# Kernel optimization log

Hardware: AMD Instinct MI355X
Metric: run time of the kernel (lower is better)

The kernel has to match this reference:

```python
import jax, jax.numpy as jnp
import numpy as np

NUM_HEADS = 8
NUM_POINTS = 9


def _bilinear_sample(img, gx, gy):
    """grid_sample, mode=bilinear, padding=zeros, align_corners=True.
    img: (B, C, H, W); gx, gy: (B, M) pixel coords. Returns (B, C, M)."""
    Bc, C, H, W = img.shape
    imgf = img.reshape(Bc, C, H * W)
    x0 = jnp.floor(gx)
    y0 = jnp.floor(gy)
    wx1 = gx - x0
    wy1 = gy - y0

    def corner(xi, yi, w):
        valid = (xi >= 0) & (xi < W) & (yi >= 0) & (yi < H)
        xi_c = jnp.clip(xi, 0, W - 1).astype(jnp.int32)
        yi_c = jnp.clip(yi, 0, H - 1).astype(jnp.int32)
        idx = yi_c * W + xi_c  # (B, M)
        g = jax.vmap(lambda im, ix: im[:, ix])(imgf, idx)  # (B, C, M)
        return g * (w * valid)[:, None, :]

    return (corner(x0, y0, (1 - wx1) * (1 - wy1))
            + corner(x0 + 1, y0, wx1 * (1 - wy1))
            + corner(x0, y0 + 1, (1 - wx1) * wy1)
            + corner(x0 + 1, y0 + 1, wx1 * wy1))


def setup_inputs() -> dict:
    key = jax.random.key(0)
    ks = jax.random.split(key, 6)
    B, Hp, Wp, T, D = 4, 64, 64, 3, 256
    N = Hp * Wp
    Hh, P = NUM_HEADS, NUM_POINTS
    x = jax.random.normal(ks[0], (B, N, T, D), dtype=jnp.float32)
    # offset/attn projections: small random (orig inits them to 0, which is degenerate for testing)
    W_off = jax.random.normal(ks[1], (D, Hh * P * 2), dtype=jnp.float32) * 0.01
    b_off = jnp.zeros((Hh * P * 2,), dtype=jnp.float32)
    W_attn = jax.random.normal(ks[2], (D, Hh * P), dtype=jnp.float32) * 0.01
    b_attn = jnp.zeros((Hh * P,), dtype=jnp.float32)
    W_v = jax.random.normal(ks[3], (D, D), dtype=jnp.float32) * 0.02
    b_v = jnp.zeros((D,), dtype=jnp.float32)
    W_o = jax.random.normal(ks[4], (D, D), dtype=jnp.float32) * 0.02
    b_o = jnp.zeros((D,), dtype=jnp.float32)
    return {"x": x, "W_off": W_off, "b_off": b_off, "W_attn": W_attn,
            "b_attn": b_attn, "W_v": W_v, "b_v": b_v, "W_o": W_o,
            "b_o": b_o, "Hp": Hp, "Wp": Wp}


def reference(x, W_off, b_off, W_attn, b_attn, W_v, b_v, W_o, b_o, Hp, Wp):
    B, N, T, D = x.shape
    Hh, P = NUM_HEADS, NUM_POINTS
    dh = D // Hh

    query = x[:, :, T // 2]  # (B, N, D) middle frame
    offset = (query @ W_off + b_off).reshape(B, N, Hh, P, 2)
    attn = jax.nn.softmax((query @ W_attn + b_attn).reshape(B, N, Hh, P), axis=-1)

    # reference points in [-1, 1], xy order (x = width coord)
    gh, gw = jnp.meshgrid(jnp.arange(Hp, dtype=jnp.float32),
                          jnp.arange(Wp, dtype=jnp.float32), indexing='ij')
    ref = jnp.stack([gw, gh], axis=-1).reshape(N, 2)
    ref = ref / jnp.asarray([Wp - 1, Hp - 1], dtype=jnp.float32) * 2 - 1

    loc = ref[None, :, None, None, :] + offset  # (B, N, H, P, 2) normalized

    value = (x @ W_v + b_v).reshape(B, N, T, Hh, dh)
    # (B, H, T, dh, N) -> (B*H*T, dh, Hp, Wp)
    val = jnp.transpose(value, (0, 3, 2, 4, 1)).reshape(B * Hh * T, dh, Hp, Wp)

    # per-(b,h) grid, shared across frames; fold T into batch of the sampler
    grid = jnp.transpose(loc, (0, 2, 1, 3, 4))  # (B, H, N, P, 2)
    grid = jnp.broadcast_to(grid[:, :, None], (B, Hh, T, N, P, 2))
    grid = grid.reshape(B * Hh * T, N * P, 2)
    gx = (grid[..., 0] + 1) * 0.5 * (Wp - 1)
    gy = (grid[..., 1] + 1) * 0.5 * (Hp - 1)

    sampled = _bilinear_sample(val, gx, gy)  # (B*H*T, dh, N*P)
    sampled = sampled.reshape(B, Hh, T, dh, N, P)

    # weighted sum over points, summed over frames
    out = jnp.einsum('bhtdnp,bnhp->bnhd', sampled, attn).reshape(B, N, D)
    return out @ W_o + b_o
```

## Files before the change

kernel.cpp:

```cpp
#include <hip/hip_runtime.h>
#include <hip/hip_bf16.h>


#define NH_ 8
#define DH_ 32
#define MM_ 16384

typedef __attribute__((ext_vector_type(8))) short bf16x8;
typedef __attribute__((ext_vector_type(4))) short bf16x4;
typedef __attribute__((ext_vector_type(4))) float f32x4;

static __device__ __forceinline__ unsigned short f2bf(float f) {
  unsigned int u = __float_as_uint(f);
  u = (u + 0x7fff + ((u >> 16) & 1)) >> 16;
  return (unsigned short)u;
}
static __device__ __forceinline__ float bf2f(unsigned short h) {
  return __uint_as_float(((unsigned int)h) << 16);
}

__global__ __launch_bounds__(256) void prep(
    const float* __restrict__ x,
    const float* __restrict__ W_off, const float* __restrict__ W_attn,
    const float* __restrict__ W_v, const float* __restrict__ W_o,
    const float* __restrict__ b_off, const float* __restrict__ b_attn,
    unsigned short* __restrict__ ash, unsigned short* __restrict__ asl,
    unsigned short* __restrict__ xmh, unsigned short* __restrict__ xml,
    unsigned short* __restrict__ wvh, unsigned short* __restrict__ wvl,
    unsigned short* __restrict__ wch, unsigned short* __restrict__ wcl,
    unsigned short* __restrict__ woh, unsigned short* __restrict__ wol,
    float* __restrict__ bcat) {
  const int bid = blockIdx.x, t = threadIdx.x;
  if (bid < 4096) {
    const int gid = bid * 256 + t;
    const int row = gid >> 6, c4 = (gid & 63) * 4;
    const float* xr = x + (size_t)row * 768 + c4;
    float4 a0 = *(const float4*)xr;
    float4 a1 = *(const float4*)(xr + 256);
    float4 a2 = *(const float4*)(xr + 512);
    float s[4] = {a0.x + a1.x + a2.x, a0.y + a1.y + a2.y,
                  a0.z + a1.z + a2.z, a0.w + a1.w + a2.w};
    float m[4] = {a1.x, a1.y, a1.z, a1.w};
    bf16x4 shv, slv, mhv, mlv;
#pragma unroll
    for (int j = 0; j < 4; ++j) {
      unsigned short h = f2bf(s[j]);
      shv[j] = (short)h; slv[j] = (short)f2bf(s[j] - bf2f(h));
      unsigned short h2 = f2bf(m[j]);
      mhv[j] = (short)h2; mlv[j] = (short)f2bf(m[j] - bf2f(h2));
    }
    const size_t o = (size_t)row * 256 + c4;
    *(bf16x4*)(ash + o) = shv;  *(bf16x4*)(asl + o) = slv;
    *(bf16x4*)(xmh + o) = mhv;  *(bf16x4*)(xml + o) = mlv;
  } else {
    const int n = bid - 4096;
    {
      float v = W_v[(size_t)t * 256 + n];
      unsigned short h = f2bf(v);
      wvh[n * 256 + t] = h; wvl[n * 256 + t] = f2bf(v - bf2f(h));
    }
    {
      float v = W_o[(size_t)t * 256 + n];
      unsigned short h = f2bf(v);
      woh[n * 256 + t] = h; wol[n * 256 + t] = f2bf(v - bf2f(h));
    }
    if (n < 216) {
      float v = (n < 144) ? W_off[(size_t)t * 144 + n] : W_attn[(size_t)t * 72 + (n - 144)];
      unsigned short h = f2bf(v);
      wch[n * 256 + t] = h; wcl[n * 256 + t] = f2bf(v - bf2f(h));
    }
    if (n == 0 && t < 216) bcat[t] = (t < 144) ? b_off[t] : b_attn[t - 144];
  }
}

__global__ __launch_bounds__(256) void mgemm01(
    const unsigned short* __restrict__ Ahi, const unsigned short* __restrict__ Alo,
    const unsigned short* __restrict__ Xmh, const unsigned short* __restrict__ Xml,
    const unsigned short* __restrict__ Wvh, const unsigned short* __restrict__ Wvl,
    const unsigned short* __restrict__ Wch, const unsigned short* __restrict__ Wcl,
    const float* __restrict__ b_v, const float* __restrict__ bcat,
    float* __restrict__ valsum, float* __restrict__ proj) {
  __shared__ unsigned short Ah[64][64], Al[64][64], Bh[128][64], Bl[128][64];
  const int mode1 = (blockIdx.y >= 2);
  const int n0 = (blockIdx.y & 1) * 128;
  const int m0 = blockIdx.x * 64;
  const int tid = threadIdx.x;
  const int wid = tid >> 6, lane = tid & 63;
  const int am = (wid >> 1) * 32, bn = (wid & 1) * 64;
  const int fr = lane & 15, kg = lane >> 4;
  const unsigned short* Asrch = mode1 ? Xmh : Ahi;
  const unsigned short* Asrcl = mode1 ? Xml : Alo;
  const unsigned short* Bth = mode1 ? Wch : Wvh;
  const unsigned short* Btl = mode1 ? Wcl : Wvl;

  f32x4 acc[2][4];
#pragma unroll
  for (int i = 0; i < 2; ++i)
#pragma unroll
    for (int j = 0; j < 4; ++j) acc[i][j] = (f32x4)(0.f);

  for (int k0 = 0; k0 < 256; k0 += 64) {
#pragma unroll
    for (int i = 0; i < 2; ++i) {
      int cid = i * 256 + tid;
      int r = cid >> 3, c = cid & 7;
      int dst = r * 64 + ((c ^ (r & 7)) * 8);
      size_t off = (size_t)(m0 + r) * 256 + k0 + c * 8;
      *(bf16x8*)(&Ah[0][0] + dst) = *(const bf16x8*)(Asrch + off);
      *(bf16x8*)(&Al[0][0] + dst) = *(const bf16x8*)(Asrcl + off);
    }
#pragma unroll
    for (int i = 0; i < 4; ++i) {
      int cid = i * 256 + tid;
      int r = cid >> 3, c = cid & 7;
      int dst = r * 64 + ((c ^ (r & 7)) * 8);
      int nrow = n0 + r;
      bf16x8 hv = (bf16x8)(short)0, lv = (bf16x8)(short)0;
      if (!mode1 || nrow < 216) {
        size_t off = (size_t)nrow * 256 + k0 + c * 8;
        hv = *(const bf16x8*)(Bth + off);
        lv = *(const bf16x8*)(Btl + off);
      }
      *(bf16x8*)(&Bh[0][0] + dst) = hv;
      *(bf16x8*)(&Bl[0][0] + dst) = lv;
    }
    __syncthreads();

#pragma unroll
    for (int ks = 0; ks < 2; ++ks) {
      const int kc = ks * 4 + kg;
      bf16x8 ah[2], al[2], bh[4], bl[4];
#pragma unroll
      for (int mi = 0; mi < 2; ++mi) {
        int m = am + mi * 16 + fr;
        int o = m * 64 + ((kc ^ (m & 7)) * 8);
        ah[mi] = *(const bf16x8*)(&Ah[0][0] + o);
        al[mi] = *(const bf16x8*)(&Al[0][0] + o);
      }
#pragma unroll
      for (int ni = 0; ni < 4; ++ni) {
        int n = bn + ni * 16 + fr;
        int o = n * 64 + ((kc ^ (n & 7)) * 8);
        bh[ni] = *(const bf16x8*)(&Bh[0][0] + o);
        bl[ni] = *(const bf16x8*)(&Bl[0][0] + o);
      }
#pragma unroll
      for (int mi = 0; mi < 2; ++mi)
#pragma unroll
        for (int ni = 0; ni < 4; ++ni) {
          acc[mi][ni] = __builtin_amdgcn_mfma_f32_16x16x32_bf16(ah[mi], bh[ni], acc[mi][ni], 0, 0, 0);
          acc[mi][ni] = __builtin_amdgcn_mfma_f32_16x16x32_bf16(ah[mi], bl[ni], acc[mi][ni], 0, 0, 0);
          acc[mi][ni] = __builtin_amdgcn_mfma_f32_16x16x32_bf16(al[mi], bh[ni], acc[mi][ni], 0, 0, 0);
        }
    }
    __syncthreads();
  }

  const int ro = kg * 4;
#pragma unroll
  for (int mi = 0; mi < 2; ++mi)
#pragma unroll
    for (int ni = 0; ni < 4; ++ni) {
      int col = n0 + bn + ni * 16 + fr;
      if (mode1 && col >= 216) continue;
      int rowb = m0 + am + mi * 16 + ro;
      float bv = mode1 ? bcat[col] : b_v[col] * 3.f;
#pragma unroll
      for (int r = 0; r < 4; ++r) {
        int grow = rowb + r;
        float v = acc[mi][ni][r] + bv;
        if (mode1) {
          proj[(size_t)grow * 216 + col] = v;
        } else {
          int b = grow >> 12, nn = grow & 4095;
          int h = col >> 5, d = col & 31;
          valsum[(((size_t)(b * NH_ + h) << 12) + nn) * DH_ + d] = v;
        }
      }
    }
}

__global__ __launch_bounds__(256) void mgemm2(
    const unsigned short* __restrict__ Ahi, const unsigned short* __restrict__ Alo,
    const unsigned short* __restrict__ Bth, const unsigned short* __restrict__ Btl,
    const float* __restrict__ bias, float* __restrict__ Cout) {
  __shared__ unsigned short Ah[64][64], Al[64][64], Bh[128][64], Bl[128][64];
  const int n0 = blockIdx.y * 128;
  const int m0 = blockIdx.x * 64;
  const int tid = threadIdx.x;
  const int wid = tid >> 6, lane = tid & 63;
  const int am = (wid >> 1) * 32, bn = (wid & 1) * 64;
  const int fr = lane & 15, kg = lane >> 4;

  f32x4 acc[2][4];
#pragma unroll
  for (int i = 0; i < 2; ++i)
#pragma unroll
    for (int j = 0; j < 4; ++j) acc[i][j] = (f32x4)(0.f);

  for (int k0 = 0; k0 < 256; k0 += 64) {
#pragma unroll
    for (int i = 0; i < 2; ++i) {
      int cid = i * 256 + tid;
      int r = cid >> 3, c = cid & 7;
      int dst = r * 64 + ((c ^ (r & 7)) * 8);
      size_t off = (size_t)(m0 + r) * 256 + k0 + c * 8;
      *(bf16x8*)(&Ah[0][0] + dst) = *(const bf16x8*)(Ahi + off);
      *(bf16x8*)(&Al[0][0] + dst) = *(const bf16x8*)(Alo + off);
    }
#pragma unroll
    for (int i = 0; i < 4; ++i) {
      int cid = i * 256 + tid;
      int r = cid >> 3, c = cid & 7;
      int dst = r * 64 + ((c ^ (r & 7)) * 8);
      size_t off = (size_t)(n0 + r) * 256 + k0 + c * 8;
      *(bf16x8*)(&Bh[0][0] + dst) = *(const bf16x8*)(Bth + off);
      *(bf16x8*)(&Bl[0][0] + dst) = *(const bf16x8*)(Btl + off);
    }
    __syncthreads();

#pragma unroll
    for (int ks = 0; ks < 2; ++ks) {
      const int kc = ks * 4 + kg;
      bf16x8 ah[2], al[2], bh[4], bl[4];
#pragma unroll
      for (int mi = 0; mi < 2; ++mi) {
        int m = am + mi * 16 + fr;
        int o = m * 64 + ((kc ^ (m & 7)) * 8);
        ah[mi] = *(const bf16x8*)(&Ah[0][0] + o);
        al[mi] = *(const bf16x8*)(&Al[0][0] + o);
      }
#pragma unroll
      for (int ni = 0; ni < 4; ++ni) {
        int n = bn + ni * 16 + fr;
        int o = n * 64 + ((kc ^ (n & 7)) * 8);
        bh[ni] = *(const bf16x8*)(&Bh[0][0] + o);
        bl[ni] = *(const bf16x8*)(&Bl[0][0] + o);
      }
#pragma unroll
      for (int mi = 0; mi < 2; ++mi)
#pragma unroll
        for (int ni = 0; ni < 4; ++ni) {
          acc[mi][ni] = __builtin_amdgcn_mfma_f32_16x16x32_bf16(ah[mi], bh[ni], acc[mi][ni], 0, 0, 0);
          acc[mi][ni] = __builtin_amdgcn_mfma_f32_16x16x32_bf16(ah[mi], bl[ni], acc[mi][ni], 0, 0, 0);
          acc[mi][ni] = __builtin_amdgcn_mfma_f32_16x16x32_bf16(al[mi], bh[ni], acc[mi][ni], 0, 0, 0);
        }
    }
    __syncthreads();
  }

  const int ro = kg * 4;
#pragma unroll
  for (int mi = 0; mi < 2; ++mi)
#pragma unroll
    for (int ni = 0; ni < 4; ++ni) {
      int col = n0 + bn + ni * 16 + fr;
      int rowb = m0 + am + mi * 16 + ro;
      float bv = bias[col];
#pragma unroll
      for (int r = 0; r < 4; ++r)
        Cout[(size_t)(rowb + r) * 256 + col] = acc[mi][ni][r] + bv;
    }
}

__global__ __launch_bounds__(256) void sample4(const float* __restrict__ valsum,
                                               const float* __restrict__ proj,
                                               unsigned short* __restrict__ ihi,
                                               unsigned short* __restrict__ ilo) {
  const int bid = blockIdx.x;
  const int wv = threadIdx.x >> 6;
  const int lane = threadIdx.x & 63;
  const int row = ((bid & 7) << 11) + ((bid >> 3) << 2) + wv;
  const int b = row >> 12, n = row & 4095;

  __shared__ int cidx[4][72][4];
  __shared__ float cw[4][72][4];
  __shared__ float sa[4][72];

  const float* pr = proj + (size_t)row * 216;
  for (int e = lane; e < 72; e += 64) {
    float ox = pr[e * 2], oy = pr[e * 2 + 1];
    float gx = (float)(n & 63) + ox * 31.5f;
    float gy = (float)(n >> 6) + oy * 31.5f;
    float fx0 = floorf(gx), fy0 = floorf(gy);
    float wx1 = gx - fx0, wy1 = gy - fy0;
    float wx0 = 1.f - wx1, wy0 = 1.f - wy1;
    int x0 = (int)fx0, y0 = (int)fy0, x1 = x0 + 1, y1 = y0 + 1;
    bool vx0 = (x0 >= 0) & (x0 < 64), vx1 = (x1 >= 0) & (x1 < 64);
    bool vy0 = (y0 >= 0) & (y0 < 64), vy1 = (y1 >= 0) & (y1 < 64);
    int x0c = min(max(x0, 0), 63), x1c = min(max(x1, 0), 63);
    int y0c = min(max(y0, 0), 63), y1c = min(max(y1, 0), 63);
    cidx[wv][e][0] = (y0c * 64 + x0c) * DH_; cw[wv][e][0] = (vx0 & vy0) ? wx0 * wy0 : 0.f;
    cidx[wv][e][1] = (y0c * 64 + x1c) * DH_; cw[wv][e][1] = (vx1 & vy0) ? wx1 * wy0 : 0.f;
    cidx[wv][e][2] = (y1c * 64 + x0c) * DH_; cw[wv][e][2] = (vx0 & vy1) ? wx0 * wy1 : 0.f;
    cidx[wv][e][3] = (y1c * 64 + x1c) * DH_; cw[wv][e][3] = (vx1 & vy1) ? wx1 * wy1 : 0.f;
  }
  if (lane < 8) {
    const float* pa = pr + 144 + lane * 9;
    float lg[9], mx = -1e30f;
#pragma unroll
    for (int p = 0; p < 9; ++p) { lg[p] = pa[p]; mx = fmaxf(mx, lg[p]); }
    float s = 0.f;
#pragma unroll
    for (int p = 0; p < 9; ++p) { lg[p] = __expf(lg[p] - mx); s += lg[p]; }
    float inv = 1.f / s;
#pragma unroll
    for (int p = 0; p < 9; ++p) sa[wv][lane * 9 + p] = lg[p] * inv;
  }
  __syncthreads();

  const int h = lane >> 3, d4 = (lane & 7) * 4;
  const float* vb = valsum + ((size_t)((b * NH_ + h) << 12)) * DH_ + d4;
  float ax = 0.f, ay = 0.f, az = 0.f, aw = 0.f;
#pragma unroll
  for (int p = 0; p < 9; ++p) {
    const int hp = h * 9 + p;
    float sx = 0.f, sy = 0.f, sz = 0.f, sw = 0.f;
#pragma unroll
    for (int c = 0; c < 4; ++c) {
      float4 v = *(const float4*)(vb + cidx[wv][hp][c]);
      float w = cw[wv][hp][c];
      sx += w * v.x; sy += w * v.y; sz += w * v.z; sw += w * v.w;
    }
    float ap = sa[wv][hp];
    ax += ap * sx; ay += ap * sy; az += ap * sz; aw += ap * sw;
  }
  float av[4] = {ax, ay, az, aw};
  bf16x4 hv, lv;
#pragma unroll
  for (int j = 0; j < 4; ++j) {
    unsigned short hh = f2bf(av[j]);
    hv[j] = (short)hh;
    lv[j] = (short)f2bf(av[j] - bf2f(hh));
  }
  const size_t o = (size_t)row * 256 + lane * 4;
  *(bf16x4*)(ihi + o) = hv;
  *(bf16x4*)(ilo + o) = lv;
}

extern "C" void kernel_launch(void* const* d_in, const int* in_sizes, int n_in,
                              void* d_out, int out_size, void* d_ws, size_t ws_size,
                              hipStream_t stream) {
  const float* x      = (const float*)d_in[0];
  const float* W_off  = (const float*)d_in[1];
  const float* b_off  = (const float*)d_in[2];
  const float* W_attn = (const float*)d_in[3];
  const float* b_attn = (const float*)d_in[4];
  const float* W_v    = (const float*)d_in[5];
  const float* b_v    = (const float*)d_in[6];
  const float* W_o    = (const float*)d_in[7];
  const float* b_o    = (const float*)d_in[8];
  float* out = (float*)d_out;

  float* valsum = (float*)d_ws;
  float* proj   = valsum + (size_t)MM_ * 256;
  float* bcat   = proj + (size_t)MM_ * 216;
  unsigned short* ash = (unsigned short*)(bcat + 256);
  unsigned short* asl = ash + (size_t)MM_ * 256;
  unsigned short* xmh = asl + (size_t)MM_ * 256;
  unsigned short* xml = xmh + (size_t)MM_ * 256;
  unsigned short* wvh = xml + (size_t)MM_ * 256;
  unsigned short* wvl = wvh + 65536;
  unsigned short* wch = wvl + 65536;
  unsigned short* wcl = wch + 55296;
  unsigned short* woh = wcl + 55296;
  unsigned short* wol = woh + 65536;
  unsigned short* ihi = ash;
  unsigned short* ilo = asl;

  prep<<<dim3(4352), dim3(256), 0, stream>>>(x, W_off, W_attn, W_v, W_o, b_off, b_attn,
                                             ash, asl, xmh, xml,
                                             wvh, wvl, wch, wcl, woh, wol, bcat);
  mgemm01<<<dim3(256, 4), dim3(256), 0, stream>>>(ash, asl, xmh, xml, wvh, wvl, wch, wcl,
                                                  b_v, bcat, valsum, proj);
  sample4<<<dim3(4096), dim3(256), 0, stream>>>(valsum, proj, ihi, ilo);
  mgemm2<<<dim3(256, 2), dim3(256), 0, stream>>>(ihi, ilo, woh, wol, b_o, out);
}
```

Before: 174.5 us.

## Prefetch GEMM tiles into registers, shrink N tile, fuse bf16 split into output GEMM

```diff
diff --git a/kernel.cpp b/kernel.cpp
--- a/kernel.cpp
+++ b/kernel.cpp
@@ -17,6 +17,16 @@
 }
 static __device__ __forceinline__ float bf2f(unsigned short h) {
   return __uint_as_float(((unsigned int)h) << 16);
+}
+static __device__ __forceinline__ void split8(const float4 f0, const float4 f1,
+                                              bf16x8& hv, bf16x8& lv) {
+  float vv[8] = {f0.x, f0.y, f0.z, f0.w, f1.x, f1.y, f1.z, f1.w};
+#pragma unroll
+  for (int j = 0; j < 8; ++j) {
+    unsigned short h = f2bf(vv[j]);
+    hv[j] = (short)h;
+    lv[j] = (short)f2bf(vv[j] - bf2f(h));
+  }
 }
 
 __global__ __launch_bounds__(256) void prep(
@@ -73,94 +83,108 @@
   }
 }
 
-__global__ __launch_bounds__(256) void mgemm01(
+__global__ __launch_bounds__(256, 4) void mgemm01(
     const unsigned short* __restrict__ Ahi, const unsigned short* __restrict__ Alo,
     const unsigned short* __restrict__ Xmh, const unsigned short* __restrict__ Xml,
     const unsigned short* __restrict__ Wvh, const unsigned short* __restrict__ Wvl,
     const unsigned short* __restrict__ Wch, const unsigned short* __restrict__ Wcl,
     const float* __restrict__ b_v, const float* __restrict__ bcat,
     float* __restrict__ valsum, float* __restrict__ proj) {
-  __shared__ unsigned short Ah[64][64], Al[64][64], Bh[128][64], Bl[128][64];
-  const int mode1 = (blockIdx.y >= 2);
-  const int n0 = (blockIdx.y & 1) * 128;
+  __shared__ unsigned short Ah[64][64], Al[64][64], Bh[64][64], Bl[64][64];
+  const int mode1 = blockIdx.y >= 4;
+  const int n0 = (blockIdx.y & 3) * 64;
   const int m0 = blockIdx.x * 64;
-  const int tid = threadIdx.x;
-  const int wid = tid >> 6, lane = tid & 63;
-  const int am = (wid >> 1) * 32, bn = (wid & 1) * 64;
+  const int tid = threadIdx.x, wid = tid >> 6, lane = tid & 63;
+  const int am = (wid >> 1) * 32, bn = (wid & 1) * 32;
   const int fr = lane & 15, kg = lane >> 4;
-  const unsigned short* Asrch = mode1 ? Xmh : Ahi;
-  const unsigned short* Asrcl = mode1 ? Xml : Alo;
-  const unsigned short* Bth = mode1 ? Wch : Wvh;
-  const unsigned short* Btl = mode1 ? Wcl : Wvl;
-
-  f32x4 acc[2][4];
+  const unsigned short* Ahs = mode1 ? Xmh : Ahi;
+  const unsigned short* Als = mode1 ? Xml : Alo;
+  const unsigned short* Bhs = mode1 ? Wch : Wvh;
+  const unsigned short* Bls = mode1 ? Wcl : Wvl;
+
+  const int r0s = tid >> 3, c0s = tid & 7;
+  const int r1s = r0s + 32;
+  const int d0s = r0s * 64 + ((c0s ^ (r0s & 7)) * 8);
+  const int d1s = r1s * 64 + ((c0s ^ (r1s & 7)) * 8);
+
+  f32x4 acc[2][2];
 #pragma unroll
   for (int i = 0; i < 2; ++i)
 #pragma unroll
-    for (int j = 0; j < 4; ++j) acc[i][j] = (f32x4)(0.f);
-
-  for (int k0 = 0; k0 < 256; k0 += 64) {
-#pragma unroll
-    for (int i = 0; i < 2; ++i) {
-      int cid = i * 256 + tid;
-      int r = cid >> 3, c = cid & 7;
-      int dst = r * 64 + ((c ^ (r & 7)) * 8);
-      size_t off = (size_t)(m0 + r) * 256 + k0 + c * 8;
-      *(bf16x8*)(&Ah[0][0] + dst) = *(const bf16x8*)(Asrch + off);
-      *(bf16x8*)(&Al[0][0] + dst) = *(const bf16x8*)(Asrcl + off);
-    }
-#pragma unroll
-    for (int i = 0; i < 4; ++i) {
-      int cid = i * 256 + tid;
-      int r = cid >> 3, c = cid & 7;
-      int dst = r * 64 + ((c ^ (r & 7)) * 8);
-      int nrow = n0 + r;
-      bf16x8 hv = (bf16x8)(short)0, lv = (bf16x8)(short)0;
-      if (!mode1 || nrow < 216) {
-        size_t off = (size_t)nrow * 256 + k0 + c * 8;
-        hv = *(const bf16x8*)(Bth + off);
-        lv = *(const bf16x8*)(Btl + off);
-      }
-      *(bf16x8*)(&Bh[0][0] + dst) = hv;
-      *(bf16x8*)(&Bl[0][0] + dst) = lv;
-    }
+    for (int j = 0; j < 2; ++j) acc[i][j] = (f32x4)(0.f);
+
+  bf16x8 pah[2], pal[2], pbh[2], pbl[2];
+
+#define LOADT01(k0)                                                          \
+  {                                                                          \
+    size_t a0 = (size_t)(m0 + r0s) * 256 + (k0) + c0s * 8;                   \
+    size_t a1 = (size_t)(m0 + r1s) * 256 + (k0) + c0s * 8;                   \
+    pah[0] = *(const bf16x8*)(Ahs + a0); pal[0] = *(const bf16x8*)(Als + a0);\
+    pah[1] = *(const bf16x8*)(Ahs + a1); pal[1] = *(const bf16x8*)(Als + a1);\
+    int nr0 = n0 + r0s, nr1 = n0 + r1s;                                      \
+    size_t b0 = (size_t)nr0 * 256 + (k0) + c0s * 8;                          \
+    size_t b1 = (size_t)nr1 * 256 + (k0) + c0s * 8;                          \
+    if (!mode1 || nr0 < 216) {                                               \
+      pbh[0] = *(const bf16x8*)(Bhs + b0); pbl[0] = *(const bf16x8*)(Bls + b0);\
+    } else { pbh[0] = (bf16x8)(short)0; pbl[0] = (bf16x8)(short)0; }         \
+    if (!mode1 || nr1 < 216) {                                               \
+      pbh[1] = *(const bf16x8*)(Bhs + b1); pbl[1] = *(const bf16x8*)(Bls + b1);\
+    } else { pbh[1] = (bf16x8)(short)0; pbl[1] = (bf16x8)(short)0; }         \
+  }
+
+#define WRITET()                                                             \
+  {                                                                          \
+    *(bf16x8*)(&Ah[0][0] + d0s) = pah[0]; *(bf16x8*)(&Al[0][0] + d0s) = pal[0];\
+    *(bf16x8*)(&Ah[0][0] + d1s) = pah[1]; *(bf16x8*)(&Al[0][0] + d1s) = pal[1];\
+    *(bf16x8*)(&Bh[0][0] + d0s) = pbh[0]; *(bf16x8*)(&Bl[0][0] + d0s) = pbl[0];\
+    *(bf16x8*)(&Bh[0][0] + d1s) = pbh[1]; *(bf16x8*)(&Bl[0][0] + d1s) = pbl[1];\
+  }
+
+#define COMPUTET()                                                           \
+  _Pragma("unroll")                                                          \
+  for (int ks = 0; ks < 2; ++ks) {                                           \
+    const int kc = ks * 4 + kg;                                              \
+    bf16x8 ah[2], al[2], bh[2], bl[2];                                       \
+    _Pragma("unroll")                                                        \
+    for (int mi = 0; mi < 2; ++mi) {                                         \
+      int m = am + mi * 16 + fr;                                             \
+      int o = m * 64 + ((kc ^ (m & 7)) * 8);                                 \
+      ah[mi] = *(const bf16x8*)(&Ah[0][0] + o);                              \
+      al[mi] = *(const bf16x8*)(&Al[0][0] + o);                              \
+    }                                                                        \
+    _Pragma("unroll")                                                        \
+    for (int ni = 0; ni < 2; ++ni) {                                         \
+      int nn = bn + ni * 16 + fr;                                            \
+      int o = nn * 64 + ((kc ^ (nn & 7)) * 8);                               \
+      bh[ni] = *(const bf16x8*)(&Bh[0][0] + o);                              \
+      bl[ni] = *(const bf16x8*)(&Bl[0][0] + o);                              \
+    }                                                                        \
+    _Pragma("unroll")                                                        \
+    for (int mi = 0; mi < 2; ++mi)                                           \
+      _Pragma("unroll")                                                      \
+      for (int ni = 0; ni < 2; ++ni) {                                       \
+        acc[mi][ni] = __builtin_amdgcn_mfma_f32_16x16x32_bf16(ah[mi], bh[ni], acc[mi][ni], 0, 0, 0);\
+        acc[mi][ni] = __builtin_amdgcn_mfma_f32_16x16x32_bf16(ah[mi], bl[ni], acc[mi][ni], 0, 0, 0);\
+        acc[mi][ni] = __builtin_amdgcn_mfma_f32_16x16x32_bf16(al[mi], bh[ni], acc[mi][ni], 0, 0, 0);\
+      }                                                                      \
+  }
+
+  LOADT01(0);
+  WRITET();
+  __syncthreads();
+#pragma unroll
+  for (int t = 0; t < 4; ++t) {
+    if (t < 3) LOADT01((t + 1) * 64);
+    COMPUTET();
     __syncthreads();
-
-#pragma unroll
-    for (int ks = 0; ks < 2; ++ks) {
-      const int kc = ks * 4 + kg;
-      bf16x8 ah[2], al[2], bh[4], bl[4];
-#pragma unroll
-      for (int mi = 0; mi < 2; ++mi) {
-        int m = am + mi * 16 + fr;
-        int o = m * 64 + ((kc ^ (m & 7)) * 8);
-        ah[mi] = *(const bf16x8*)(&Ah[0][0] + o);
-        al[mi] = *(const bf16x8*)(&Al[0][0] + o);
-      }
-#pragma unroll
-      for (int ni = 0; ni < 4; ++ni) {
-        int n = bn + ni * 16 + fr;
-        int o = n * 64 + ((kc ^ (n & 7)) * 8);
-        bh[ni] = *(const bf16x8*)(&Bh[0][0] + o);
-        bl[ni] = *(const bf16x8*)(&Bl[0][0] + o);
-      }
-#pragma unroll
-      for (int mi = 0; mi < 2; ++mi)
-#pragma unroll
-        for (int ni = 0; ni < 4; ++ni) {
-          acc[mi][ni] = __builtin_amdgcn_mfma_f32_16x16x32_bf16(ah[mi], bh[ni], acc[mi][ni], 0, 0, 0);
-          acc[mi][ni] = __builtin_amdgcn_mfma_f32_16x16x32_bf16(ah[mi], bl[ni], acc[mi][ni], 0, 0, 0);
-          acc[mi][ni] = __builtin_amdgcn_mfma_f32_16x16x32_bf16(al[mi], bh[ni], acc[mi][ni], 0, 0, 0);
-        }
-    }
-    __syncthreads();
+    if (t < 3) { WRITET(); __syncthreads(); }
   }
 
   const int ro = kg * 4;
 #pragma unroll
   for (int mi = 0; mi < 2; ++mi)
 #pragma unroll
-    for (int ni = 0; ni < 4; ++ni) {
+    for (int ni = 0; ni < 2; ++ni) {
       int col = n0 + bn + ni * 16 + fr;
       if (mode1 && col >= 216) continue;
       int rowb = m0 + am + mi * 16 + ro;
@@ -172,88 +196,110 @@
         if (mode1) {
           proj[(size_t)grow * 216 + col] = v;
         } else {
-          int b = grow >> 12, nn = grow & 4095;
+          int b = grow >> 12, nn2 = grow & 4095;
           int h = col >> 5, d = col & 31;
-          valsum[(((size_t)(b * NH_ + h) << 12) + nn) * DH_ + d] = v;
+          valsum[(((size_t)(b * NH_ + h) << 12) + nn2) * DH_ + d] = v;
         }
       }
     }
-}
-
-__global__ __launch_bounds__(256) void mgemm2(
-    const unsigned short* __restrict__ Ahi, const unsigned short* __restrict__ Alo,
-    const unsigned short* __restrict__ Bth, const unsigned short* __restrict__ Btl,
+#undef LOADT01
+#undef WRITET
+#undef COMPUTET
+}
+
+__global__ __launch_bounds__(256, 4) void mgemm2(
+    const float* __restrict__ Af, 
+    const unsigned short* __restrict__ Bhs, const unsigned short* __restrict__ Bls,
     const float* __restrict__ bias, float* __restrict__ Cout) {
-  __shared__ unsigned short Ah[64][64], Al[64][64], Bh[128][64], Bl[128][64];
-  const int n0 = blockIdx.y * 128;
+  __shared__ unsigned short Ah[64][64], Al[64][64], Bh[64][64], Bl[64][64];
+  const int n0 = blockIdx.y * 64;
   const int m0 = blockIdx.x * 64;
-  const int tid = threadIdx.x;
-  const int wid = tid >> 6, lane = tid & 63;
-  const int am = (wid >> 1) * 32, bn = (wid & 1) * 64;
+  const int tid = threadIdx.x, wid = tid >> 6, lane = tid & 63;
+  const int am = (wid >> 1) * 32, bn = (wid & 1) * 32;
   const int fr = lane & 15, kg = lane >> 4;
 
-  f32x4 acc[2][4];
+  const int r0s = tid >> 3, c0s = tid & 7;
+  const int r1s = r0s + 32;
+  const int d0s = r0s * 64 + ((c0s ^ (r0s & 7)) * 8);
+  const int d1s = r1s * 64 + ((c0s ^ (r1s & 7)) * 8);
+
+  f32x4 acc[2][2];
 #pragma unroll
   for (int i = 0; i < 2; ++i)
 #pragma unroll
-    for (int j = 0; j < 4; ++j) acc[i][j] = (f32x4)(0.f);
-
-  for (int k0 = 0; k0 < 256; k0 += 64) {
-#pragma unroll
-    for (int i = 0; i < 2; ++i) {
-      int cid = i * 256 + tid;
-      int r = cid >> 3, c = cid & 7;
-      int dst = r * 64 + ((c ^ (r & 7)) * 8);
-      size_t off = (size_t)(m0 + r) * 256 + k0 + c * 8;
-      *(bf16x8*)(&Ah[0][0] + dst) = *(const bf16x8*)(Ahi + off);
-      *(bf16x8*)(&Al[0][0] + dst) = *(const bf16x8*)(Alo + off);
-    }
-#pragma unroll
-    for (int i = 0; i < 4; ++i) {
-      int cid = i * 256 + tid;
-      int r = cid >> 3, c = cid & 7;
-      int dst = r * 64 + ((c ^ (r & 7)) * 8);
-      size_t off = (size_t)(n0 + r) * 256 + k0 + c * 8;
-      *(bf16x8*)(&Bh[0][0] + dst) = *(const bf16x8*)(Bth + off);
-      *(bf16x8*)(&Bl[0][0] + dst) = *(const bf16x8*)(Btl + off);
-    }
+    for (int j = 0; j < 2; ++j) acc[i][j] = (f32x4)(0.f);
+
+  float4 pf[2][2];
+  bf16x8 pbh[2], pbl[2];
+
+#define LOADT2(k0)                                                           \
+  {                                                                          \
+    const float* s0 = Af + (size_t)(m0 + r0s) * 256 + (k0) + c0s * 8;        \
+    const float* s1 = Af + (size_t)(m0 + r1s) * 256 + (k0) + c0s * 8;        \
+    pf[0][0] = *(const float4*)s0; pf[0][1] = *(const float4*)(s0 + 4);      \
+    pf[1][0] = *(const float4*)s1; pf[1][1] = *(const float4*)(s1 + 4);      \
+    size_t b0 = (size_t)(n0 + r0s) * 256 + (k0) + c0s * 8;                   \
+    size_t b1 = (size_t)(n0 + r1s) * 256 + (k0) + c0s * 8;                   \
+    pbh[0] = *(const bf16x8*)(Bhs + b0); pbl[0] = *(const bf16x8*)(Bls + b0);\
+    pbh[1] = *(const bf16x8*)(Bhs + b1); pbl[1] = *(const bf16x8*)(Bls + b1);\
+  }
+
+#define WRITET2()                                                            \
+  {                                                                          \
+    bf16x8 hv, lv;                                                           \
+    split8(pf[0][0], pf[0][1], hv, lv);                                      \
+    *(bf16x8*)(&Ah[0][0] + d0s) = hv; *(bf16x8*)(&Al[0][0] + d0s) = lv;      \
+    split8(pf[1][0], pf[1][1], hv, lv);                                      \
+    *(bf16x8*)(&Ah[0][0] + d1s) = hv; *(bf16x8*)(&Al[0][0] + d1s) = lv;      \
+    *(bf16x8*)(&Bh[0][0] + d0s) = pbh[0]; *(bf16x8*)(&Bl[0][0] + d0s) = pbl[0];\
+    *(bf16x8*)(&Bh[0][0] + d1s) = pbh[1]; *(bf16x8*)(&Bl[0][0] + d1s) = pbl[1];\
+  }
+
+#define COMPUTET2()                                                          \
+  _Pragma("unroll")                                                          \
+  for (int ks = 0; ks < 2; ++ks) {                                           \
+    const int kc = ks * 4 + kg;                                              \
+    bf16x8 ah[2], al[2], bh[2], bl[2];                                       \
+    _Pragma("unroll")                                                        \
+    for (int mi = 0; mi < 2; ++mi) {                                         \
+      int m = am + mi * 16 + fr;                                             \
+      int o = m * 64 + ((kc ^ (m & 7)) * 8);                                 \
+      ah[mi] = *(const bf16x8*)(&Ah[0][0] + o);                              \
+      al[mi] = *(const bf16x8*)(&Al[0][0] + o);                              \
+    }                                                                        \
+    _Pragma("unroll")                                                        \
+    for (int ni = 0; ni < 2; ++ni) {                                         \
+      int nn = bn + ni * 16 + fr;                                            \
+      int o = nn * 64 + ((kc ^ (nn & 7)) * 8);                               \
+      bh[ni] = *(const bf16x8*)(&Bh[0][0] + o);                              \
+      bl[ni] = *(const bf16x8*)(&Bl[0][0] + o);                              \
+    }                                                                        \
+    _Pragma("unroll")                                                        \
+    for (int mi = 0; mi < 2; ++mi)                                           \
+      _Pragma("unroll")                                                      \
+      for (int ni = 0; ni < 2; ++ni) {                                       \
+        acc[mi][ni] = __builtin_amdgcn_mfma_f32_16x16x32_bf16(ah[mi], bh[ni], acc[mi][ni], 0, 0, 0);\
+        acc[mi][ni] = __builtin_amdgcn_mfma_f32_16x16x32_bf16(ah[mi], bl[ni], acc[mi][ni], 0, 0, 0);\
+        acc[mi][ni] = __builtin_amdgcn_mfma_f32_16x16x32_bf16(al[mi], bh[ni], acc[mi][ni], 0, 0, 0);\
+      }                                                                      \
+  }
+
+  LOADT2(0);
+  WRITET2();
+  __syncthreads();
+#pragma unroll
+  for (int t = 0; t < 4; ++t) {
+    if (t < 3) LOADT2((t + 1) * 64);
+    COMPUTET2();
     __syncthreads();
-
-#pragma unroll
-    for (int ks = 0; ks < 2; ++ks) {
-      const int kc = ks * 4 + kg;
-      bf16x8 ah[2], al[2], bh[4], bl[4];
-#pragma unroll
-      for (int mi = 0; mi < 2; ++mi) {
-        int m = am + mi * 16 + fr;
-        int o = m * 64 + ((kc ^ (m & 7)) * 8);
-        ah[mi] = *(const bf16x8*)(&Ah[0][0] + o);
-        al[mi] = *(const bf16x8*)(&Al[0][0] + o);
-      }
-#pragma unroll
-      for (int ni = 0; ni < 4; ++ni) {
-        int n = bn + ni * 16 + fr;
-        int o = n * 64 + ((kc ^ (n & 7)) * 8);
-        bh[ni] = *(const bf16x8*)(&Bh[0][0] + o);
-        bl[ni] = *(const bf16x8*)(&Bl[0][0] + o);
-      }
-#pragma unroll
-      for (int mi = 0; mi < 2; ++mi)
-#pragma unroll
-        for (int ni = 0; ni < 4; ++ni) {
-          acc[mi][ni] = __builtin_amdgcn_mfma_f32_16x16x32_bf16(ah[mi], bh[ni], acc[mi][ni], 0, 0, 0);
-          acc[mi][ni] = __builtin_amdgcn_mfma_f32_16x16x32_bf16(ah[mi], bl[ni], acc[mi][ni], 0, 0, 0);
-          acc[mi][ni] = __builtin_amdgcn_mfma_f32_16x16x32_bf16(al[mi], bh[ni], acc[mi][ni], 0, 0, 0);
-        }
-    }
-    __syncthreads();
+    if (t < 3) { WRITET2(); __syncthreads(); }
   }
 
   const int ro = kg * 4;
 #pragma unroll
   for (int mi = 0; mi < 2; ++mi)
 #pragma unroll
-    for (int ni = 0; ni < 4; ++ni) {
+    for (int ni = 0; ni < 2; ++ni) {
       int col = n0 + bn + ni * 16 + fr;
       int rowb = m0 + am + mi * 16 + ro;
       float bv = bias[col];
@@ -261,23 +307,39 @@
       for (int r = 0; r < 4; ++r)
         Cout[(size_t)(rowb + r) * 256 + col] = acc[mi][ni][r] + bv;
     }
-}
+#undef LOADT2
+#undef WRITET2
+#undef COMPUTET2
+}
+
+struct IW { int idx; float w; };
 
 __global__ __launch_bounds__(256) void sample4(const float* __restrict__ valsum,
                                                const float* __restrict__ proj,
-                                               unsigned short* __restrict__ ihi,
-                                               unsigned short* __restrict__ ilo) {
+                                               float* __restrict__ inter) {
   const int bid = blockIdx.x;
   const int wv = threadIdx.x >> 6;
   const int lane = threadIdx.x & 63;
   const int row = ((bid & 7) << 11) + ((bid >> 3) << 2) + wv;
   const int b = row >> 12, n = row & 4095;
 
-  __shared__ int cidx[4][72][4];
-  __shared__ float cw[4][72][4];
-  __shared__ float sa[4][72];
+  __shared__ IW cwi[4][72][4];
+  __shared__ float sap[4][76];
 
   const float* pr = proj + (size_t)row * 216;
+  if (lane < 8) {
+    const float* pa = pr + 144 + lane * 9;
+    float lg[9], mx = -1e30f;
+#pragma unroll
+    for (int p = 0; p < 9; ++p) { lg[p] = pa[p]; mx = fmaxf(mx, lg[p]); }
+    float s = 0.f;
+#pragma unroll
+    for (int p = 0; p < 9; ++p) { lg[p] = __expf(lg[p] - mx); s += lg[p]; }
+    float inv = 1.f / s;
+#pragma unroll
+    for (int p = 0; p < 9; ++p) sap[wv][lane * 9 + p] = lg[p] * inv;
+  }
+  __syncthreads();
   for (int e = lane; e < 72; e += 64) {
     float ox = pr[e * 2], oy = pr[e * 2 + 1];
     float gx = (float)(n & 63) + ox * 31.5f;
@@ -290,52 +352,37 @@
     bool vy0 = (y0 >= 0) & (y0 < 64), vy1 = (y1 >= 0) & (y1 < 64);
     int x0c = min(max(x0, 0), 63), x1c = min(max(x1, 0), 63);
     int y0c = min(max(y0, 0), 63), y1c = min(max(y1, 0), 63);
-    cidx[wv][e][0] = (y0c * 64 + x0c) * DH_; cw[wv][e][0] = (vx0 & vy0) ? wx0 * wy0 : 0.f;
-    cidx[wv][e][1] = (y0c * 64 + x1c) * DH_; cw[wv][e][1] = (vx1 & vy0) ? wx1 * wy0 : 0.f;
-    cidx[wv][e][2] = (y1c * 64 + x0c) * DH_; cw[wv][e][2] = (vx0 & vy1) ? wx0 * wy1 : 0.f;
-    cidx[wv][e][3] = (y1c * 64 + x1c) * DH_; cw[wv][e][3] = (vx1 & vy1) ? wx1 * wy1 : 0.f;
-  }
-  if (lane < 8) {
-    const float* pa = pr + 144 + lane * 9;
-    float lg[9], mx = -1e30f;
-#pragma unroll
-    for (int p = 0; p < 9; ++p) { lg[p] = pa[p]; mx = fmaxf(mx, lg[p]); }
-    float s = 0.f;
-#pragma unroll
-    for (int p = 0; p < 9; ++p) { lg[p] = __expf(lg[p] - mx); s += lg[p]; }
-    float inv = 1.f / s;
-#pragma unroll
-    for (int p = 0; p < 9; ++p) sa[wv][lane * 9 + p] = lg[p] * inv;
+    const float a = sap[wv][e];
+    cwi[wv][e][0] = IW{(y0c * 64 + x0c) * DH_, (vx0 & vy0) ? wx0 * wy0 * a : 0.f};
+    cwi[wv][e][1] = IW{(y0c * 64 + x1c) * DH_, (vx1 & vy0) ? wx1 * wy0 * a : 0.f};
+    cwi[wv][e][2] = IW{(y1c * 64 + x0c) * DH_, (vx0 & vy1) ? wx0 * wy1 * a : 0.f};
+    cwi[wv][e][3] = IW{(y1c * 64 + x1c) * DH_, (vx1 & vy1) ? wx1 * wy1 * a : 0.f};
   }
   __syncthreads();
 
   const int h = lane >> 3, d4 = (lane & 7) * 4;
-  const float* vb = valsum + ((size_t)((b * NH_ + h) << 12)) * DH_ + d4;
+  const float* vb = valsum + (((size_t)(b * NH_ + h)) << 12) * DH_ + d4;
   float ax = 0.f, ay = 0.f, az = 0.f, aw = 0.f;
 #pragma unroll
-  for (int p = 0; p < 9; ++p) {
-    const int hp = h * 9 + p;
-    float sx = 0.f, sy = 0.f, sz = 0.f, sw = 0.f;
-#pragma unroll
-    for (int c = 0; c < 4; ++c) {
-      float4 v = *(const float4*)(vb + cidx[wv][hp][c]);
-      float w = cw[wv][hp][c];
-      sx += w * v.x; sy += w * v.y; sz += w * v.z; sw += w * v.w;
-    }
-    float ap = sa[wv][hp];
-    ax += ap * sx; ay += ap * sy; az += ap * sz; aw += ap * sw;
-  }
-  float av[4] = {ax, ay, az, aw};
-  bf16x4 hv, lv;
-#pragma unroll
-  for (int j = 0; j < 4; ++j) {
-    unsigned short hh = f2bf(av[j]);
-    hv[j] = (short)hh;
-    lv[j] = (short)f2bf(av[j] - bf2f(hh));
-  }
-  const size_t o = (size_t)row * 256 + lane * 4;
-  *(bf16x4*)(ihi + o) = hv;
-  *(bf16x4*)(ilo + o) = lv;
+  for (int pb = 0; pb < 9; pb += 3) {
+    float4 v[12]; float w[12];
+#pragma unroll
+    for (int q = 0; q < 3; ++q) {
+      const int hp = h * 9 + pb + q;
+#pragma unroll
+      for (int c = 0; c < 4; ++c) {
+        IW e = cwi[wv][hp][c];
+        v[q * 4 + c] = *(const float4*)(vb + e.idx);
+        w[q * 4 + c] = e.w;
+      }
+    }
+#pragma unroll
+    for (int j = 0; j < 12; ++j) {
+      ax += w[j] * v[j].x; ay += w[j] * v[j].y;
+      az += w[j] * v[j].z; aw += w[j] * v[j].w;
+    }
+  }
+  *(float4*)(inter + (size_t)row * 256 + h * DH_ + d4) = make_float4(ax, ay, az, aw);
 }
 
 extern "C" void kernel_launch(void* const* d_in, const int* in_sizes, int n_in,
@@ -365,14 +412,13 @@
   unsigned short* wcl = wch + 55296;
   unsigned short* woh = wcl + 55296;
   unsigned short* wol = woh + 65536;
-  unsigned short* ihi = ash;
-  unsigned short* ilo = asl;
+  float* inter = (float*)ash;
 
   prep<<<dim3(4352), dim3(256), 0, stream>>>(x, W_off, W_attn, W_v, W_o, b_off, b_attn,
                                              ash, asl, xmh, xml,
                                              wvh, wvl, wch, wcl, woh, wol, bcat);
-  mgemm01<<<dim3(256, 4), dim3(256), 0, stream>>>(ash, asl, xmh, xml, wvh, wvl, wch, wcl,
+  mgemm01<<<dim3(256, 8), dim3(256), 0, stream>>>(ash, asl, xmh, xml, wvh, wvl, wch, wcl,
                                                   b_v, bcat, valsum, proj);
-  sample4<<<dim3(4096), dim3(256), 0, stream>>>(valsum, proj, ihi, ilo);
-  mgemm2<<<dim3(256, 2), dim3(256), 0, stream>>>(ihi, ilo, woh, wol, b_o, out);
-}
+  sample4<<<dim3(4096), dim3(256), 0, stream>>>(valsum, proj, inter);
+  mgemm2<<<dim3(256, 4), dim3(256), 0, stream>>>(inter, woh, wol, b_o, out);
+}
```

New measurement: 166.3 us. -4.8%, faster.
